# Kernel optimization log

Hardware: AMD Instinct MI355X
Metric: run time of the kernel (lower is better)

The kernel has to match this reference:

```python
import jax, jax.numpy as jnp
import numpy as np

IN_DIM, OUT_DIM, EDGE_DIM = 128, 128, 16
N_NODES, N_EDGES = 20000, 640000


def setup_inputs() -> dict:
    key = jax.random.key(0)
    ks = jax.random.split(key, 16)
    s = lambda fan_in: 1.0 / np.sqrt(fan_in)
    h = jax.random.normal(ks[0], (N_NODES, IN_DIM), dtype=jnp.float32)
    edge_index = jax.random.randint(ks[1], (2, N_EDGES), 0, N_NODES, dtype=jnp.int32)
    edge_attr = jax.random.normal(ks[2], (N_EDGES, EDGE_DIM), dtype=jnp.float32)
    flags = jnp.ones((N_NODES, 1), dtype=jnp.float32)
    edge_mask = jnp.ones((N_EDGES, 1), dtype=jnp.float32)
    din_msg = 2 * IN_DIM + EDGE_DIM
    din_node = IN_DIM + OUT_DIM
    params = {
        'W_m1': jax.random.uniform(ks[3], (din_msg, OUT_DIM), jnp.float32, -s(din_msg), s(din_msg)),
        'b_m1': jnp.zeros((OUT_DIM,), jnp.float32),
        'W_m2': jax.random.uniform(ks[4], (OUT_DIM, OUT_DIM), jnp.float32, -s(OUT_DIM), s(OUT_DIM)),
        'b_m2': jnp.zeros((OUT_DIM,), jnp.float32),
        'W_a': jax.random.uniform(ks[5], (OUT_DIM, 1), jnp.float32, -s(OUT_DIM), s(OUT_DIM)),
        'b_a': jnp.zeros((1,), jnp.float32),
        'W_n1': jax.random.uniform(ks[6], (din_node, OUT_DIM), jnp.float32, -s(din_node), s(din_node)),
        'b_n1': jnp.zeros((OUT_DIM,), jnp.float32),
        'W_n2': jax.random.uniform(ks[7], (OUT_DIM, OUT_DIM), jnp.float32, -s(OUT_DIM), s(OUT_DIM)),
        'b_n2': jnp.zeros((OUT_DIM,), jnp.float32),
    }
    return {'h': h, 'edge_index': edge_index, 'edge_attr': edge_attr,
            'flags': flags, 'edge_mask': edge_mask, **params}


def reference(h, edge_index, edge_attr, flags, edge_mask,
              W_m1, b_m1, W_m2, b_m2, W_a, b_a, W_n1, b_n1, W_n2, b_n2):
    row, col = edge_index[0], edge_index[1]
    # gather endpoints and run edge MLP
    msg = jnp.concatenate([h[row], h[col], edge_attr], axis=1)  # [E, 2*in+edge]
    msg = jax.nn.silu(msg @ W_m1 + b_m1)
    msg = jax.nn.silu(msg @ W_m2 + b_m2)                        # [E, out]
    att = jax.nn.sigmoid(msg @ W_a + b_a)                       # [E, 1]
    msg = msg * att * edge_mask
    # scatter-add into source nodes (aggregation 'sum', norm factor 1)
    agg = jax.ops.segment_sum(msg, row, num_segments=h.shape[0])  # [N, out]
    agg = jnp.concatenate([h, agg], axis=1)                       # [N, in+out]
    upd = jax.nn.silu(agg @ W_n1 + b_n1) @ W_n2 + b_n2
    return (h + upd) * flags
```

## Files before the change

### kernel.cpp

```cpp
#include <hip/hip_runtime.h>
#include <math.h>

#define E_TOT   640000
#define NN      20000
#define DIM     128
#define EDGE_DIM 16

typedef float f32x4 __attribute__((ext_vector_type(4)));
typedef float f32x2 __attribute__((ext_vector_type(2)));
typedef short s16x8 __attribute__((ext_vector_type(8)));
typedef unsigned u32x4 __attribute__((ext_vector_type(4)));
typedef __bf16 bfx8 __attribute__((ext_vector_type(8)));

__device__ __forceinline__ unsigned short f2bf(float f) {
    unsigned u = __builtin_bit_cast(unsigned, f);
    u += 0x7fffu + ((u >> 16) & 1u);
    return (unsigned short)(u >> 16);
}
__device__ __forceinline__ unsigned cvt_pk_bf16(float lo, float hi) {
    unsigned r;
    asm("v_cvt_pk_bf16_f32 %0, %1, %2" : "=v"(r) : "v"(lo), "v"(hi));
    return r;
}
__device__ __forceinline__ float bf_lo(unsigned u) {
    return __builtin_bit_cast(float, u << 16);
}
__device__ __forceinline__ float bf_hi(unsigned u) {
    return __builtin_bit_cast(float, u & 0xffff0000u);
}
__device__ __forceinline__ f32x2 bf2(unsigned u) {
    f32x2 r; r.x = bf_lo(u); r.y = bf_hi(u); return r;
}
__device__ __forceinline__ float fast_exp2(float x) {
    float r; asm("v_exp_f32 %0, %1" : "=v"(r) : "v"(x)); return r;
}
__device__ __forceinline__ float fast_rcp(float x) {
    float r; asm("v_rcp_f32 %0, %1" : "=v"(r) : "v"(x)); return r;
}
#define LOG2E 1.44269504f
__device__ __forceinline__ float silu_f(float x) {
    return x * fast_rcp(1.0f + fast_exp2(-LOG2E * x));
}
__device__ __forceinline__ float sigmoid_f(float x) {
    return fast_rcp(1.0f + fast_exp2(-LOG2E * x));
}
__device__ __forceinline__ f32x2 silu2(f32x2 x) {
    f32x2 nx = x * (-LOG2E);
    f32x2 e; e.x = fast_exp2(nx.x); e.y = fast_exp2(nx.y);
    f32x2 d = e + 1.0f;
    f32x2 rc; rc.x = fast_rcp(d.x); rc.y = fast_rcp(d.y);
    return x * rc;
}

#define MFMA16(a, b, c) __builtin_amdgcn_mfma_f32_16x16x32_bf16( \
    __builtin_bit_cast(bfx8, (a)), __builtin_bit_cast(bfx8, (b)), (c), 0, 0, 0)

__device__ __forceinline__ void pack_w(const float* __restrict__ W,
                                       unsigned short* __restrict__ Wp,
                                       int K, int id) {
    int t   = id & 7;
    int pos = (id >> 3) & 127;
    int sg  = id >> 10;
    int qq = pos & 15, f = pos >> 4;
    int col = (f >> 1) * 32 + 2 * qq + (f & 1);
    int k = sg * 8 + t;
    Wp[id] = (k < K) ? f2bf(W[(size_t)k * DIM + col]) : (unsigned short)0;
}

__global__ void prep_all_kernel(const float* __restrict__ h,
                                unsigned short* __restrict__ h_bf,
                                const float* __restrict__ Wm1,
                                const float* __restrict__ Wm2,
                                const float* __restrict__ Wn1,
                                const float* __restrict__ Wn2,
                                unsigned short* __restrict__ W1rp,
                                unsigned short* __restrict__ W1cp,
                                unsigned short* __restrict__ W1ep,
                                unsigned short* __restrict__ W2p,
                                unsigned short* __restrict__ Wn1p,
                                unsigned short* __restrict__ Wn2p,
                                float* __restrict__ agg,
                                int* __restrict__ cnts) {
    const int blk = blockIdx.x;
    const int tid = threadIdx.x;
    if (blk < 2500) {
        int i = blk * 256 + tid;
        float4 v = reinterpret_cast<const float4*>(h)[i];
        unsigned short* d = h_bf + i * 4;
        d[0] = f2bf(v.x); d[1] = f2bf(v.y); d[2] = f2bf(v.z); d[3] = f2bf(v.w);
    } else if (blk < 2564) {
        pack_w(Wm1, W1rp, 128, (blk - 2500) * 256 + tid);
    } else if (blk < 2628) {
        pack_w(Wm1 + 128 * DIM, W1cp, 128, (blk - 2564) * 256 + tid);
    } else if (blk < 2644) {
        pack_w(Wm1 + 256 * DIM, W1ep, 16, (blk - 2628) * 256 + tid);
    } else if (blk < 2708) {
        pack_w(Wm2, W2p, 128, (blk - 2644) * 256 + tid);
    } else if (blk < 2836) {
        pack_w(Wn1, Wn1p, 256, (blk - 2708) * 256 + tid);
    } else if (blk < 2900) {
        pack_w(Wn2, Wn2p, 128, (blk - 2836) * 256 + tid);
    } else if (blk < 5400) {
        int i = (blk - 2900) * 256 + tid;
        reinterpret_cast<f32x4*>(agg)[i] = (f32x4)0.f;
    } else {
        int i = (blk - 5400) * 256 + tid;
        if (i < NN) cnts[i] = 0;
    }
}

template<bool SORTED>
__global__ __launch_bounds__(256) void hist_proj_kernel(
    const int* __restrict__ ei, int* __restrict__ cnts,
    const unsigned short* __restrict__ h_bf,
    const unsigned short* __restrict__ W1rp,
    const unsigned short* __restrict__ W1cp,
    unsigned* __restrict__ P1r, unsigned* __restrict__ P1c)
{
    const int blk = blockIdx.x;
    const int tid = threadIdx.x;

    if (SORTED && blk < 2500) {
        int e = blk * 256 + tid;
        if (e < E_TOT) atomicAdd(&cnts[ei[e]], 1);
        return;
    }

    const int pblk = SORTED ? (blk - 2500) : blk;
    const int wv   = tid >> 6;
    const int lane = tid & 63;
    const int q    = lane & 15;
    const int g    = lane >> 4;
    const int n0w  = pblk * 64 + wv * 16;
    const int nq   = n0w + q;
    const int nqc  = (nq < NN) ? nq : (NN - 1);

    s16x8 av[4];
    #pragma unroll
    for (int s = 0; s < 4; ++s)
        av[s] = *reinterpret_cast<const s16x8*>(
            h_bf + (size_t)nqc * DIM + s * 32 + g * 8);

    #pragma unroll
    for (int T = 0; T < 2; ++T) {
        const unsigned short* Wp = T ? W1cp : W1rp;
        unsigned* P = T ? P1c : P1r;
        f32x4 acc[8];
        #pragma unroll
        for (int f = 0; f < 8; ++f) acc[f] = (f32x4)0.f;
        #pragma unroll
        for (int s = 0; s < 4; ++s)
            #pragma unroll
            for (int f = 0; f < 8; ++f) {
                s16x8 b = *reinterpret_cast<const s16x8*>(
                    Wp + ((s * 4 + g) * DIM + f * 16 + q) * 8);
                acc[f] = MFMA16(av[s], b, acc[f]);
            }
        #pragma unroll
        for (int r = 0; r < 4; ++r) {
            int n = n0w + g * 4 + r;
            if (n < NN) {
                u32x4 o;
                #pragma unroll
                for (int a = 0; a < 4; ++a)
                    o[a] = cvt_pk_bf16(acc[2 * a][r], acc[2 * a + 1][r]);
                *reinterpret_cast<u32x4*>(P + (size_t)n * 64 + q * 4) = o;
            }
        }
    }
}

__global__ __launch_bounds__(1024) void scan_kernel(int* __restrict__ counts) {
    __shared__ int s[1024];
    const int tid = threadIdx.x;
    const int CH = 20;
    int base = tid * CH;
    int loc[CH];
    int sum = 0;
    #pragma unroll
    for (int i = 0; i < CH; ++i) {
        int idx = base + i;
        loc[i] = (idx < NN) ? counts[idx] : 0;
        sum += loc[i];
    }
    s[tid] = sum;
    __syncthreads();
    for (int off = 1; off < 1024; off <<= 1) {
        int v = (tid >= off) ? s[tid - off] : 0;
        __syncthreads();
        s[tid] += v;
        __syncthreads();
    }
    int run = s[tid] - sum;
    #pragma unroll
    for (int i = 0; i < CH; ++i) {
        int idx = base + i;
        if (idx < NN) counts[idx] = run;
        run += loc[i];
    }
}

__global__ void scatter_kernel(const int* __restrict__ ei, int* __restrict__ cursor,
                               int* __restrict__ eidS, unsigned short* __restrict__ rowS) {
    int e = blockIdx.x * blockDim.x + threadIdx.x;
    if (e < E_TOT) {
        int r = ei[e];
        int p = atomicAdd(&cursor[r], 1);
        eidS[p] = e;
        rowS[p] = (unsigned short)r;
    }
}

template<bool SORTED>
__global__ __launch_bounds__(256, 2) void edge_kernel(
    const unsigned* __restrict__ P1r,
    const unsigned* __restrict__ P1c,
    const int* __restrict__ ei,
    const int* __restrict__ eidS,
    const unsigned short* __restrict__ rowS,
    const float* __restrict__ ea,
    const float* __restrict__ emask,
    const unsigned short* __restrict__ W1ep,
    const float* __restrict__ bm1,
    const unsigned short* __restrict__ W2p,
    const float* __restrict__ bm2,
    const float* __restrict__ Wa, const float* __restrict__ ba,
    float* __restrict__ agg)
{
    __shared__ __align__(16) unsigned char s_u[4][16384];

    const int tid  = threadIdx.x;
    const int wv   = tid >> 6;
    const int lane = tid & 63;
    const int q    = lane & 15;
    const int g    = lane >> 4;

    const int nwg = gridDim.x;
    const int xcd = blockIdx.x & 7;
    const int loc = blockIdx.x >> 3;
    const int qq  = nwg >> 3, rr = nwg & 7;
    const int tile = (xcd < rr) ? (xcd * (qq + 1) + loc)
                                : (rr * (qq + 1) + (xcd - rr) * qq + loc);
    const int e0w = tile * 256 + wv * 64;

    const int   eidl = SORTED ? eidS[e0w + lane] : (e0w + lane);
    const int   rowl = SORTED ? (int)rowS[e0w + lane] : ei[eidl];
    const int   coll = ei[E_TOT + eidl];
    const float mskl = emask[eidl];

    const u32x4* P1r4 = reinterpret_cast<const u32x4*>(P1r);
    const u32x4* P1c4 = reinterpret_cast<const u32x4*>(P1c);

    s16x8 eav[4];
    #pragma unroll
    for (int mi = 0; mi < 4; ++mi) {
        int eid = __shfl(eidl, mi * 16 + q);
        eav[mi] = (s16x8)0;
        if (g < 2) {
            const float4* pe = reinterpret_cast<const float4*>(
                ea + (size_t)eid * EDGE_DIM + g * 8);
            float4 u = pe[0], v = pe[1];
            u32x4 pk;
            pk[0] = cvt_pk_bf16(u.x, u.y); pk[1] = cvt_pk_bf16(u.z, u.w);
            pk[2] = cvt_pk_bf16(v.x, v.y); pk[3] = cvt_pk_bf16(v.z, v.w);
            eav[mi] = __builtin_bit_cast(s16x8, pk);
        }
    }

    s16x8 w1e[8];
    #pragma unroll
    for (int f = 0; f < 8; ++f)
        w1e[f] = *reinterpret_cast<const s16x8*>(
            W1ep + ((size_t)g * DIM + f * 16 + q) * 8);

    f32x2 b1v[4];
    #pragma unroll
    for (int a = 0; a < 4; ++a)
        b1v[a] = *reinterpret_cast<const f32x2*>(bm1 + a * 32 + 2 * q);

    unsigned char* sw = s_u[wv];

    u32x4 pr[4], pc[4];
    #pragma unroll
    for (int r = 0; r < 4; ++r) {
        int e = g * 4 + r;
        pr[r] = P1r4[(size_t)__shfl(rowl, e) * 16 + q];
        pc[r] = P1c4[(size_t)__shfl(coll, e) * 16 + q];
    }

    #pragma unroll
    for (int mi = 0; mi < 4; ++mi) {
        f32x4 a1[8];
        #pragma unroll
        for (int f = 0; f < 8; ++f) a1[f] = (f32x4)0.f;
        #pragma unroll
        for (int f = 0; f < 8; ++f) a1[f] = MFMA16(eav[mi], w1e[f], a1[f]);

        u32x4 prn[4], pcn[4];
        if (mi < 3) {
            #pragma unroll
            for (int r = 0; r < 4; ++r) {
                int e = (mi + 1) * 16 + g * 4 + r;
                prn[r] = P1r4[(size_t)__shfl(rowl, e) * 16 + q];
                pcn[r] = P1c4[(size_t)__shfl(coll, e) * 16 + q];
            }
        }

        #pragma unroll
        for (int r = 0; r < 4; ++r) {
            int e = mi * 16 + g * 4 + r;
            unsigned sx = (unsigned)((e & 7) << 4);
            #pragma unroll
            for (int a = 0; a < 4; ++a) {
                f32x2 t; t.x = a1[2 * a][r]; t.y = a1[2 * a + 1][r];
                t = t + bf2(pr[r][a]) + bf2(pc[r][a]) + b1v[a];
                f32x2 s = silu2(t);
                *reinterpret_cast<unsigned*>(
                    sw + e * 256 + ((a * 64 + q * 4) ^ sx)) = cvt_pk_bf16(s.x, s.y);
            }
        }
        #pragma unroll
        for (int r = 0; r < 4; ++r) { pr[r] = prn[r]; pc[r] = pcn[r]; }
    }

    f32x4 acc2[4][8];
    #pragma unroll
    for (int mi = 0; mi < 4; ++mi)
        #pragma unroll
        for (int f = 0; f < 8; ++f) acc2[mi][f] = (f32x4)0.f;

    #pragma unroll
    for (int s = 0; s < 4; ++s) {
        s16x8 bf[8];
        #pragma unroll
        for (int f = 0; f < 8; ++f)
            bf[f] = *reinterpret_cast<const s16x8*>(
                W2p + ((s * 4 + g) * DIM + f * 16 + q) * 8);
        s16x8 av[4];
        #pragma unroll
        for (int mi = 0; mi < 4; ++mi) {
            int e = mi * 16 + q;
            av[mi] = *reinterpret_cast<const s16x8*>(
                sw + e * 256 + ((s * 64 + g * 16) ^ ((q & 7) << 4)));
        }
        #pragma unroll
        for (int mi = 0; mi < 4; ++mi)
            #pragma unroll
            for (int f = 0; f < 8; ++f) acc2[mi][f] = MFMA16(av[mi], bf[f], acc2[mi][f]);
    }

    unsigned* smsg = reinterpret_cast<unsigned*>(sw);
    {
        f32x2 b2v[4], wav[4];
        #pragma unroll
        for (int a = 0; a < 4; ++a) {
            b2v[a] = *reinterpret_cast<const f32x2*>(bm2 + a * 32 + 2 * q);
            wav[a] = *reinterpret_cast<const f32x2*>(Wa  + a * 32 + 2 * q);
        }
        const float ba0 = ba[0];
        #pragma unroll
        for (int mi = 0; mi < 4; ++mi)
            #pragma unroll
            for (int r = 0; r < 4; ++r) {
                f32x2 pd = (f32x2)0.f;
                f32x2 vv[4];
                #pragma unroll
                for (int a = 0; a < 4; ++a) {
                    f32x2 t; t.x = acc2[mi][2 * a][r]; t.y = acc2[mi][2 * a + 1][r];
                    t = t + b2v[a];
                    vv[a] = silu2(t);
                    pd = pd + vv[a] * wav[a];
                }
                float p = pd.x + pd.y;
                p += __shfl_xor(p, 1);
                p += __shfl_xor(p, 2);
                p += __shfl_xor(p, 4);
                p += __shfl_xor(p, 8);
                int e = mi * 16 + g * 4 + r;
                float mk = __shfl(mskl, e);
                float sc = sigmoid_f(p + ba0) * mk;
                unsigned sx = ((unsigned)(e & 4)) << 2;
                #pragma unroll
                for (int a = 0; a < 4; ++a) {
                    f32x2 m = vv[a] * sc;
                    smsg[e * 64 + ((a * 16 + q) ^ sx)] = cvt_pk_bf16(m.x, m.y);
                }
            }
    }

    {
        const int c = lane;
        f32x2 s = (f32x2)0.f;
        int prow = __builtin_amdgcn_readlane(rowl, 0);
        for (int jb = 0; jb < 64; jb += 8) {
            unsigned v[8];
            #pragma unroll
            for (int k = 0; k < 8; ++k)
                v[k] = smsg[(jb + k) * 64 + (c ^ (((jb + k) & 4) << 2))];
            #pragma unroll
            for (int k = 0; k < 8; ++k) {
                int rj = __builtin_amdgcn_readlane(rowl, jb + k);
                if (rj != prow) {
                    float* dst = agg + (size_t)prow * DIM + (c >> 4) * 32 + 2 * (c & 15);
                    atomicAdd(dst, s.x);
                    atomicAdd(dst + 1, s.y);
                    s = (f32x2)0.f; prow = rj;
                }
                s = s + bf2(v[k]);
            }
        }
        float* dst = agg + (size_t)prow * DIM + (c >> 4) * 32 + 2 * (c & 15);
        atomicAdd(dst, s.x);
        atomicAdd(dst + 1, s.y);
    }
}

__global__ __launch_bounds__(256, 4) void node_kernel(
    const unsigned short* __restrict__ h_bf,
    const float* __restrict__ agg,
    const float* __restrict__ h,
    const float* __restrict__ flags,
    const unsigned short* __restrict__ Wn1p,
    const float* __restrict__ bn1,
    const unsigned short* __restrict__ Wn2p,
    const float* __restrict__ bn2,
    float* __restrict__ out)
{
    __shared__ __align__(16) unsigned char s_u[4][4352];

    const int tid  = threadIdx.x;
    const int wv   = tid >> 6;
    const int lane = tid & 63;
    const int q    = lane & 15;
    const int g    = lane >> 4;
    const int n0w  = blockIdx.x * 64 + wv * 16;

    const int nq  = n0w + q;
    const int nqc = (nq < NN) ? nq : (NN - 1);

    float4 au[4], avv[4];
    #pragma unroll
    for (int s = 0; s < 4; ++s) {
        const float4* pa = reinterpret_cast<const float4*>(
            agg + (size_t)nqc * DIM + s * 32 + g * 8);
        au[s] = pa[0]; avv[s] = pa[1];
    }
    s16x8 ah[4];
    #pragma unroll
    for (int s = 0; s < 4; ++s)
        ah[s] = *reinterpret_cast<const s16x8*>(
            h_bf + (size_t)nqc * DIM + s * 32 + g * 8);

    f32x4 acc[8];
    #pragma unroll
    for (int f = 0; f < 8; ++f) acc[f] = (f32x4)0.f;

    #pragma unroll
    for (int s = 0; s < 4; ++s) {
        #pragma unroll
        for (int f = 0; f < 8; ++f) {
            s16x8 b = *reinterpret_cast<const s16x8*>(
                Wn1p + ((s * 4 + g) * DIM + f * 16 + q) * 8);
            acc[f] = MFMA16(ah[s], b, acc[f]);
        }
    }
    #pragma unroll
    for (int s = 4; s < 8; ++s) {
        float4 u = au[s - 4], v = avv[s - 4];
        u32x4 pk;
        pk[0] = cvt_pk_bf16(u.x, u.y); pk[1] = cvt_pk_bf16(u.z, u.w);
        pk[2] = cvt_pk_bf16(v.x, v.y); pk[3] = cvt_pk_bf16(v.z, v.w);
        s16x8 a = __builtin_bit_cast(s16x8, pk);
        #pragma unroll
        for (int f = 0; f < 8; ++f) {
            s16x8 b = *reinterpret_cast<const s16x8*>(
                Wn1p + ((s * 4 + g) * DIM + f * 16 + q) * 8);
            acc[f] = MFMA16(a, b, acc[f]);
        }
    }

    unsigned char* sw = s_u[wv];
    {
        #pragma unroll
        for (int aa = 0; aa < 4; ++aa) {
            f32x2 bp = *reinterpret_cast<const f32x2*>(bn1 + aa * 32 + 2 * q);
            #pragma unroll
            for (int r = 0; r < 4; ++r) {
                f32x2 t; t.x = acc[2 * aa][r]; t.y = acc[2 * aa + 1][r];
                f32x2 s = silu2(t + bp);
                *reinterpret_cast<unsigned*>(
                    sw + (g * 4 + r) * 272 + aa * 64 + 4 * q) = cvt_pk_bf16(s.x, s.y);
            }
        }
    }

    f32x4 acc2[8];
    #pragma unroll
    for (int f = 0; f < 8; ++f) acc2[f] = (f32x4)0.f;

    #pragma unroll
    for (int s = 0; s < 4; ++s) {
        s16x8 a = *reinterpret_cast<const s16x8*>(sw + q * 272 + s * 64 + g * 16);
        #pragma unroll
        for (int f = 0; f < 8; ++f) {
            s16x8 b = *reinterpret_cast<const s16x8*>(
                Wn2p + ((s * 4 + g) * DIM + f * 16 + q) * 8);
            acc2[f] = MFMA16(a, b, acc2[f]);
        }
    }

    {
        #pragma unroll
        for (int r = 0; r < 4; ++r) {
            int n = n0w + 4 * g + r;
            if (n < NN) {
                float fl = flags[n];
                #pragma unroll
                for (int aa = 0; aa < 4; ++aa) {
                    f32x2 b2 = *reinterpret_cast<const f32x2*>(bn2 + aa * 32 + 2 * q);
                    size_t b = (size_t)n * DIM + aa * 32 + 2 * q;
                    f32x2 hv = *reinterpret_cast<const f32x2*>(h + b);
                    f32x2 t; t.x = acc2[2 * aa][r]; t.y = acc2[2 * aa + 1][r];
                    f32x2 o = (hv + t + b2) * fl;
                    *reinterpret_cast<f32x2*>(out + b) = o;
                }
            }
        }
    }
}

extern "C" void kernel_launch(void* const* d_in, const int* in_sizes, int n_in,
                              void* d_out, int out_size, void* d_ws, size_t ws_size,
                              hipStream_t stream) {
    const float* h     = (const float*)d_in[0];
    const int*   ei    = (const int*)  d_in[1];
    const float* ea    = (const float*)d_in[2];
    const float* flags = (const float*)d_in[3];
    const float* emask = (const float*)d_in[4];
    const float* Wm1   = (const float*)d_in[5];
    const float* bm1   = (const float*)d_in[6];
    const float* Wm2   = (const float*)d_in[7];
    const float* bm2   = (const float*)d_in[8];
    const float* Wa    = (const float*)d_in[9];
    const float* ba    = (const float*)d_in[10];
    const float* Wn1   = (const float*)d_in[11];
    const float* bn1   = (const float*)d_in[12];
    const float* Wn2   = (const float*)d_in[13];
    const float* bn2   = (const float*)d_in[14];
    float* out = (float*)d_out;

    char* ws = (char*)d_ws;
    float*          agg   = (float*)         (ws);
    unsigned short* h_bf  = (unsigned short*)(ws + 10240000);
    unsigned short* W1rp  = (unsigned short*)(ws + 15360000);
    unsigned short* W1cp  = (unsigned short*)(ws + 15392768);
    unsigned short* W1ep  = (unsigned short*)(ws + 15425536);
    unsigned short* W2p   = (unsigned short*)(ws + 15433728);
    unsigned short* Wn1p  = (unsigned short*)(ws + 15466496);
    unsigned short* Wn2p  = (unsigned short*)(ws + 15532032);
    int*            cnts  = (int*)           (ws + 15564800);
    int*            eidS  = (int*)           (ws + 15644800);
    unsigned short* rowS  = (unsigned short*)(ws + 18204800);
    unsigned*       P1r   = (unsigned*)      (ws + 19484800);
    unsigned*       P1c   = (unsigned*)      (ws + 24604800);
    const size_t WS_NEED = 29724800;

    const bool sorted = (ws_size >= WS_NEED);

    prep_all_kernel<<<5479, 256, 0, stream>>>(h, h_bf, Wm1, Wm2, Wn1, Wn2,
                                              W1rp, W1cp, W1ep, W2p, Wn1p, Wn2p,
                                              agg, cnts);

    if (sorted) {
        hist_proj_kernel<true><<<2813, 256, 0, stream>>>(
            ei, cnts, h_bf, W1rp, W1cp, P1r, P1c);
        scan_kernel<<<1, 1024, 0, stream>>>(cnts);
        scatter_kernel<<<(E_TOT + 255) / 256, 256, 0, stream>>>(ei, cnts, eidS, rowS);
        edge_kernel<true><<<E_TOT / 256, 256, 0, stream>>>(
            P1r, P1c, ei, eidS, rowS, ea, emask, W1ep, bm1, W2p, bm2, Wa, ba, agg);
    } else {
        hist_proj_kernel<false><<<313, 256, 0, stream>>>(
            ei, cnts, h_bf, W1rp, W1cp, P1r, P1c);
        edge_kernel<false><<<E_TOT / 256, 256, 0, stream>>>(
            P1r, P1c, ei, eidS, rowS, ea, emask, W1ep, bm1, W2p, bm2, Wa, ba, agg);
    }

    node_kernel<<<(NN + 63) / 64, 256, 0, stream>>>(h_bf, agg, h, flags,
                                                    Wn1p, bn1, Wn2p, bn2, out);
}
```

Before: 227.7 us.

## Fuse histogram into pack, fuse scatter into projection, split node kernel waves

New measurement: 262.1 us. 15.1% more time.

```diff
diff --git a/kernel.cpp b/kernel.cpp
--- a/kernel.cpp
+++ b/kernel.cpp
@@ -38,9 +38,6 @@
     float r; asm("v_rcp_f32 %0, %1" : "=v"(r) : "v"(x)); return r;
 }
 #define LOG2E 1.44269504f
-__device__ __forceinline__ float silu_f(float x) {
-    return x * fast_rcp(1.0f + fast_exp2(-LOG2E * x));
-}
 __device__ __forceinline__ float sigmoid_f(float x) {
     return fast_rcp(1.0f + fast_exp2(-LOG2E * x));
 }
@@ -67,27 +64,24 @@
     Wp[id] = (k < K) ? f2bf(W[(size_t)k * DIM + col]) : (unsigned short)0;
 }
 
-__global__ void prep_all_kernel(const float* __restrict__ h,
-                                unsigned short* __restrict__ h_bf,
-                                const float* __restrict__ Wm1,
-                                const float* __restrict__ Wm2,
-                                const float* __restrict__ Wn1,
-                                const float* __restrict__ Wn2,
-                                unsigned short* __restrict__ W1rp,
-                                unsigned short* __restrict__ W1cp,
-                                unsigned short* __restrict__ W1ep,
-                                unsigned short* __restrict__ W2p,
-                                unsigned short* __restrict__ Wn1p,
-                                unsigned short* __restrict__ Wn2p,
-                                float* __restrict__ agg,
-                                int* __restrict__ cnts) {
+__global__ void hist_pack_kernel(const int* __restrict__ ei,
+                                 int* __restrict__ cnts,
+                                 const float* __restrict__ Wm1,
+                                 const float* __restrict__ Wm2,
+                                 const float* __restrict__ Wn1,
+                                 const float* __restrict__ Wn2,
+                                 unsigned short* __restrict__ W1rp,
+                                 unsigned short* __restrict__ W1cp,
+                                 unsigned short* __restrict__ W1ep,
+                                 unsigned short* __restrict__ W2p,
+                                 unsigned short* __restrict__ Wn1p,
+                                 unsigned short* __restrict__ Wn2p,
+                                 float* __restrict__ agg) {
     const int blk = blockIdx.x;
     const int tid = threadIdx.x;
     if (blk < 2500) {
-        int i = blk * 256 + tid;
-        float4 v = reinterpret_cast<const float4*>(h)[i];
-        unsigned short* d = h_bf + i * 4;
-        d[0] = f2bf(v.x); d[1] = f2bf(v.y); d[2] = f2bf(v.z); d[3] = f2bf(v.w);
+        int e = blk * 256 + tid;
+        if (e < E_TOT) atomicAdd(&cnts[ei[e]], 1);
     } else if (blk < 2564) {
         pack_w(Wm1, W1rp, 128, (blk - 2500) * 256 + tid);
     } else if (blk < 2628) {
@@ -100,19 +94,48 @@
         pack_w(Wn1, Wn1p, 256, (blk - 2708) * 256 + tid);
     } else if (blk < 2900) {
         pack_w(Wn2, Wn2p, 128, (blk - 2836) * 256 + tid);
-    } else if (blk < 5400) {
+    } else {
         int i = (blk - 2900) * 256 + tid;
         reinterpret_cast<f32x4*>(agg)[i] = (f32x4)0.f;
-    } else {
-        int i = (blk - 5400) * 256 + tid;
-        if (i < NN) cnts[i] = 0;
+    }
+}
+
+__global__ __launch_bounds__(1024) void scan_kernel(int* __restrict__ counts) {
+    __shared__ int s[1024];
+    const int tid = threadIdx.x;
+    const int CH = 20;
+    int base = tid * CH;
+    int loc[CH];
+    int sum = 0;
+    #pragma unroll
+    for (int i = 0; i < CH; ++i) {
+        int idx = base + i;
+        loc[i] = (idx < NN) ? counts[idx] : 0;
+        sum += loc[i];
+    }
+    s[tid] = sum;
+    __syncthreads();
+    for (int off = 1; off < 1024; off <<= 1) {
+        int v = (tid >= off) ? s[tid - off] : 0;
+        __syncthreads();
+        s[tid] += v;
+        __syncthreads();
+    }
+    int run = s[tid] - sum;
+    #pragma unroll
+    for (int i = 0; i < CH; ++i) {
+        int idx = base + i;
+        if (idx < NN) counts[idx] = run;
+        run += loc[i];
     }
 }
 
 template<bool SORTED>
-__global__ __launch_bounds__(256) void hist_proj_kernel(
-    const int* __restrict__ ei, int* __restrict__ cnts,
-    const unsigned short* __restrict__ h_bf,
+__global__ __launch_bounds__(256) void prep_scatter_proj_kernel(
+    const float* __restrict__ h,
+    unsigned short* __restrict__ h_bf,
+    const int* __restrict__ ei, int* __restrict__ cursor,
+    int* __restrict__ eidS, unsigned short* __restrict__ rowS,
     const unsigned short* __restrict__ W1rp,
     const unsigned short* __restrict__ W1cp,
     unsigned* __restrict__ P1r, unsigned* __restrict__ P1c)
@@ -120,13 +143,25 @@
     const int blk = blockIdx.x;
     const int tid = threadIdx.x;
 
-    if (SORTED && blk < 2500) {
-        int e = blk * 256 + tid;
-        if (e < E_TOT) atomicAdd(&cnts[ei[e]], 1);
+    if (blk < 2500) {
+        int i = blk * 256 + tid;
+        float4 v = reinterpret_cast<const float4*>(h)[i];
+        unsigned short* d = h_bf + i * 4;
+        d[0] = f2bf(v.x); d[1] = f2bf(v.y); d[2] = f2bf(v.z); d[3] = f2bf(v.w);
         return;
     }
-
-    const int pblk = SORTED ? (blk - 2500) : blk;
+    if (SORTED && blk < 5000) {
+        int e = (blk - 2500) * 256 + tid;
+        if (e < E_TOT) {
+            int r = ei[e];
+            int p = atomicAdd(&cursor[r], 1);
+            eidS[p] = e;
+            rowS[p] = (unsigned short)r;
+        }
+        return;
+    }
+
+    const int pblk = SORTED ? (blk - 5000) : (blk - 2500);
     const int wv   = tid >> 6;
     const int lane = tid & 63;
     const int q    = lane & 15;
@@ -137,9 +172,15 @@
 
     s16x8 av[4];
     #pragma unroll
-    for (int s = 0; s < 4; ++s)
-        av[s] = *reinterpret_cast<const s16x8*>(
-            h_bf + (size_t)nqc * DIM + s * 32 + g * 8);
+    for (int s = 0; s < 4; ++s) {
+        const float4* ph = reinterpret_cast<const float4*>(
+            h + (size_t)nqc * DIM + s * 32 + g * 8);
+        float4 u = ph[0], v = ph[1];
+        u32x4 pk;
+        pk[0] = cvt_pk_bf16(u.x, u.y); pk[1] = cvt_pk_bf16(u.z, u.w);
+        pk[2] = cvt_pk_bf16(v.x, v.y); pk[3] = cvt_pk_bf16(v.z, v.w);
+        av[s] = __builtin_bit_cast(s16x8, pk);
+    }
 
     #pragma unroll
     for (int T = 0; T < 2; ++T) {
@@ -167,47 +208,6 @@
                 *reinterpret_cast<u32x4*>(P + (size_t)n * 64 + q * 4) = o;
             }
         }
-    }
-}
-
-__global__ __launch_bounds__(1024) void scan_kernel(int* __restrict__ counts) {
-    __shared__ int s[1024];
-    const int tid = threadIdx.x;
-    const int CH = 20;
-    int base = tid * CH;
-    int loc[CH];
-    int sum = 0;
-    #pragma unroll
-    for (int i = 0; i < CH; ++i) {
-        int idx = base + i;
-        loc[i] = (idx < NN) ? counts[idx] : 0;
-        sum += loc[i];
-    }
-    s[tid] = sum;
-    __syncthreads();
-    for (int off = 1; off < 1024; off <<= 1) {
-        int v = (tid >= off) ? s[tid - off] : 0;
-        __syncthreads();
-        s[tid] += v;
-        __syncthreads();
-    }
-    int run = s[tid] - sum;
-    #pragma unroll
-    for (int i = 0; i < CH; ++i) {
-        int idx = base + i;
-        if (idx < NN) counts[idx] = run;
-        run += loc[i];
-    }
-}
-
-__global__ void scatter_kernel(const int* __restrict__ ei, int* __restrict__ cursor,
-                               int* __restrict__ eidS, unsigned short* __restrict__ rowS) {
-    int e = blockIdx.x * blockDim.x + threadIdx.x;
-    if (e < E_TOT) {
-        int r = ei[e];
-        int p = atomicAdd(&cursor[r], 1);
-        eidS[p] = e;
-        rowS[p] = (unsigned short)r;
     }
 }
 
@@ -251,6 +251,16 @@
     const u32x4* P1r4 = reinterpret_cast<const u32x4*>(P1r);
     const u32x4* P1c4 = reinterpret_cast<const u32x4*>(P1c);
 
+    u32x4 pr[4][4], pc[4][4];
+    #pragma unroll
+    for (int mi = 0; mi < 4; ++mi)
+        #pragma unroll
+        for (int r = 0; r < 4; ++r) {
+            int e = mi * 16 + g * 4 + r;
+            pr[mi][r] = P1r4[(size_t)__shfl(rowl, e) * 16 + q];
+            pc[mi][r] = P1c4[(size_t)__shfl(coll, e) * 16 + q];
+        }
+
     s16x8 eav[4];
     #pragma unroll
     for (int mi = 0; mi < 4; ++mi) {
@@ -280,14 +290,6 @@
 
     unsigned char* sw = s_u[wv];
 
-    u32x4 pr[4], pc[4];
-    #pragma unroll
-    for (int r = 0; r < 4; ++r) {
-        int e = g * 4 + r;
-        pr[r] = P1r4[(size_t)__shfl(rowl, e) * 16 + q];
-        pc[r] = P1c4[(size_t)__shfl(coll, e) * 16 + q];
-    }
-
     #pragma unroll
     for (int mi = 0; mi < 4; ++mi) {
         f32x4 a1[8];
@@ -295,16 +297,6 @@
         for (int f = 0; f < 8; ++f) a1[f] = (f32x4)0.f;
         #pragma unroll
         for (int f = 0; f < 8; ++f) a1[f] = MFMA16(eav[mi], w1e[f], a1[f]);
-
-        u32x4 prn[4], pcn[4];
-        if (mi < 3) {
-            #pragma unroll
-            for (int r = 0; r < 4; ++r) {
-                int e = (mi + 1) * 16 + g * 4 + r;
-                prn[r] = P1r4[(size_t)__shfl(rowl, e) * 16 + q];
-                pcn[r] = P1c4[(size_t)__shfl(coll, e) * 16 + q];
-            }
-        }
 
         #pragma unroll
         for (int r = 0; r < 4; ++r) {
@@ -313,14 +305,12 @@
             #pragma unroll
             for (int a = 0; a < 4; ++a) {
                 f32x2 t; t.x = a1[2 * a][r]; t.y = a1[2 * a + 1][r];
-                t = t + bf2(pr[r][a]) + bf2(pc[r][a]) + b1v[a];
+                t = t + bf2(pr[mi][r][a]) + bf2(pc[mi][r][a]) + b1v[a];
                 f32x2 s = silu2(t);
                 *reinterpret_cast<unsigned*>(
                     sw + e * 256 + ((a * 64 + q * 4) ^ sx)) = cvt_pk_bf16(s.x, s.y);
             }
         }
-        #pragma unroll
-        for (int r = 0; r < 4; ++r) { pr[r] = prn[r]; pc[r] = pcn[r]; }
     }
 
     f32x4 acc2[4][8];
@@ -426,14 +416,16 @@
     const float* __restrict__ bn2,
     float* __restrict__ out)
 {
-    __shared__ __align__(16) unsigned char s_u[4][4352];
+    __shared__ __align__(16) unsigned char s_u[2][4352];
 
     const int tid  = threadIdx.x;
     const int wv   = tid >> 6;
     const int lane = tid & 63;
     const int q    = lane & 15;
     const int g    = lane >> 4;
-    const int n0w  = blockIdx.x * 64 + wv * 16;
+    const int grp  = wv >> 1;
+    const int half = wv & 1;
+    const int n0w  = blockIdx.x * 32 + grp * 16;
 
     const int nq  = n0w + q;
     const int nqc = (nq < NN) ? nq : (NN - 1);
@@ -451,16 +443,16 @@
         ah[s] = *reinterpret_cast<const s16x8*>(
             h_bf + (size_t)nqc * DIM + s * 32 + g * 8);
 
-    f32x4 acc[8];
-    #pragma unroll
-    for (int f = 0; f < 8; ++f) acc[f] = (f32x4)0.f;
+    f32x4 acc[4];
+    #pragma unroll
+    for (int f = 0; f < 4; ++f) acc[f] = (f32x4)0.f;
 
     #pragma unroll
     for (int s = 0; s < 4; ++s) {
         #pragma unroll
-        for (int f = 0; f < 8; ++f) {
+        for (int f = 0; f < 4; ++f) {
             s16x8 b = *reinterpret_cast<const s16x8*>(
-                Wn1p + ((s * 4 + g) * DIM + f * 16 + q) * 8);
+                Wn1p + ((s * 4 + g) * DIM + (half * 4 + f) * 16 + q) * 8);
             acc[f] = MFMA16(ah[s], b, acc[f]);
         }
     }
@@ -472,39 +464,41 @@
         pk[2] = cvt_pk_bf16(v.x, v.y); pk[3] = cvt_pk_bf16(v.z, v.w);
         s16x8 a = __builtin_bit_cast(s16x8, pk);
         #pragma unroll
-        for (int f = 0; f < 8; ++f) {
+        for (int f = 0; f < 4; ++f) {
             s16x8 b = *reinterpret_cast<const s16x8*>(
-                Wn1p + ((s * 4 + g) * DIM + f * 16 + q) * 8);
+                Wn1p + ((s * 4 + g) * DIM + (half * 4 + f) * 16 + q) * 8);
             acc[f] = MFMA16(a, b, acc[f]);
         }
     }
 
-    unsigned char* sw = s_u[wv];
+    unsigned char* sg_ = s_u[grp];
     {
         #pragma unroll
-        for (int aa = 0; aa < 4; ++aa) {
+        for (int a = 0; a < 2; ++a) {
+            int aa = half * 2 + a;
             f32x2 bp = *reinterpret_cast<const f32x2*>(bn1 + aa * 32 + 2 * q);
             #pragma unroll
             for (int r = 0; r < 4; ++r) {
-                f32x2 t; t.x = acc[2 * aa][r]; t.y = acc[2 * aa + 1][r];
+                f32x2 t; t.x = acc[2 * a][r]; t.y = acc[2 * a + 1][r];
                 f32x2 s = silu2(t + bp);
                 *reinterpret_cast<unsigned*>(
-                    sw + (g * 4 + r) * 272 + aa * 64 + 4 * q) = cvt_pk_bf16(s.x, s.y);
-            }
-        }
-    }
-
-    f32x4 acc2[8];
-    #pragma unroll
-    for (int f = 0; f < 8; ++f) acc2[f] = (f32x4)0.f;
+                    sg_ + (g * 4 + r) * 272 + aa * 64 + 4 * q) = cvt_pk_bf16(s.x, s.y);
+            }
+        }
+    }
+    __syncthreads();
+
+    f32x4 acc2[4];
+    #pragma unroll
+    for (int f = 0; f < 4; ++f) acc2[f] = (f32x4)0.f;
 
     #pragma unroll
     for (int s = 0; s < 4; ++s) {
-        s16x8 a = *reinterpret_cast<const s16x8*>(sw + q * 272 + s * 64 + g * 16);
-        #pragma unroll
-        for (int f = 0; f < 8; ++f) {
+        s16x8 a = *reinterpret_cast<const s16x8*>(sg_ + q * 272 + s * 64 + g * 16);
+        #pragma unroll
+        for (int f = 0; f < 4; ++f) {
             s16x8 b = *reinterpret_cast<const s16x8*>(
-                Wn2p + ((s * 4 + g) * DIM + f * 16 + q) * 8);
+                Wn2p + ((s * 4 + g) * DIM + (half * 4 + f) * 16 + q) * 8);
             acc2[f] = MFMA16(a, b, acc2[f]);
         }
     }
@@ -516,11 +510,12 @@
             if (n < NN) {
                 float fl = flags[n];
                 #pragma unroll
-                for (int aa = 0; aa < 4; ++aa) {
+                for (int a = 0; a < 2; ++a) {
+                    int aa = half * 2 + a;
                     f32x2 b2 = *reinterpret_cast<const f32x2*>(bn2 + aa * 32 + 2 * q);
                     size_t b = (size_t)n * DIM + aa * 32 + 2 * q;
                     f32x2 hv = *reinterpret_cast<const f32x2*>(h + b);
-                    f32x2 t; t.x = acc2[2 * aa][r]; t.y = acc2[2 * aa + 1][r];
+                    f32x2 t; t.x = acc2[2 * a][r]; t.y = acc2[2 * a + 1][r];
                     f32x2 o = (hv + t + b2) * fl;
                     *reinterpret_cast<f32x2*>(out + b) = o;
                 }
@@ -567,24 +562,27 @@
 
     const bool sorted = (ws_size >= WS_NEED);
 
-    prep_all_kernel<<<5479, 256, 0, stream>>>(h, h_bf, Wm1, Wm2, Wn1, Wn2,
-                                              W1rp, W1cp, W1ep, W2p, Wn1p, Wn2p,
-                                              agg, cnts);
-
     if (sorted) {
-        hist_proj_kernel<true><<<2813, 256, 0, stream>>>(
-            ei, cnts, h_bf, W1rp, W1cp, P1r, P1c);
+        hipMemsetAsync(cnts, 0, NN * sizeof(int), stream);
+        hist_pack_kernel<<<5400, 256, 0, stream>>>(
+            ei, cnts, Wm1, Wm2, Wn1, Wn2,
+            W1rp, W1cp, W1ep, W2p, Wn1p, Wn2p, agg);
         scan_kernel<<<1, 1024, 0, stream>>>(cnts);
-        scatter_kernel<<<(E_TOT + 255) / 256, 256, 0, stream>>>(ei, cnts, eidS, rowS);
+        prep_scatter_proj_kernel<true><<<5313, 256, 0, stream>>>(
+            h, h_bf, ei, cnts, eidS, rowS, W1rp, W1cp, P1r, P1c);
         edge_kernel<true><<<E_TOT / 256, 256, 0, stream>>>(
             P1r, P1c, ei, eidS, rowS, ea, emask, W1ep, bm1, W2p, bm2, Wa, ba, agg);
     } else {
-        hist_proj_kernel<false><<<313, 256, 0, stream>>>(
-            ei, cnts, h_bf, W1rp, W1cp, P1r, P1c);
+        hipMemsetAsync(cnts, 0, NN * sizeof(int), stream);
+        hist_pack_kernel<<<5400, 256, 0, stream>>>(
+            ei, cnts, Wm1, Wm2, Wn1, Wn2,
+            W1rp, W1cp, W1ep, W2p, Wn1p, Wn2p, agg);
+        prep_scatter_proj_kernel<false><<<2813, 256, 0, stream>>>(
+            h, h_bf, ei, cnts, eidS, rowS, W1rp, W1cp, P1r, P1c);
         edge_kernel<false><<<E_TOT / 256, 256, 0, stream>>>(
             P1r, P1c, ei, eidS, rowS, ea, emask, W1ep, bm1, W2p, bm2, Wa, ba, agg);
     }
 
-    node_kernel<<<(NN + 63) / 64, 256, 0, stream>>>(h_bf, agg, h, flags,
+    node_kernel<<<(NN + 31) / 32, 256, 0, stream>>>(h_bf, agg, h, flags,
                                                     Wn1p, bn1, Wn2p, bn2, out);
 }
```

## Reshuffle prep stages: fold histogram into weight-pack kernel, fuse scan with projection

Applied to the files above, without the earlier changes.

Result: faster. 220.0 us (-3.4%).

```diff
diff --git a/kernel.cpp b/kernel.cpp
--- a/kernel.cpp
+++ b/kernel.cpp
@@ -38,9 +38,6 @@
     float r; asm("v_rcp_f32 %0, %1" : "=v"(r) : "v"(x)); return r;
 }
 #define LOG2E 1.44269504f
-__device__ __forceinline__ float silu_f(float x) {
-    return x * fast_rcp(1.0f + fast_exp2(-LOG2E * x));
-}
 __device__ __forceinline__ float sigmoid_f(float x) {
     return fast_rcp(1.0f + fast_exp2(-LOG2E * x));
 }
@@ -67,27 +64,24 @@
     Wp[id] = (k < K) ? f2bf(W[(size_t)k * DIM + col]) : (unsigned short)0;
 }
 
-__global__ void prep_all_kernel(const float* __restrict__ h,
-                                unsigned short* __restrict__ h_bf,
-                                const float* __restrict__ Wm1,
-                                const float* __restrict__ Wm2,
-                                const float* __restrict__ Wn1,
-                                const float* __restrict__ Wn2,
-                                unsigned short* __restrict__ W1rp,
-                                unsigned short* __restrict__ W1cp,
-                                unsigned short* __restrict__ W1ep,
-                                unsigned short* __restrict__ W2p,
-                                unsigned short* __restrict__ Wn1p,
-                                unsigned short* __restrict__ Wn2p,
-                                float* __restrict__ agg,
-                                int* __restrict__ cnts) {
+__global__ void hist_pack_kernel(const int* __restrict__ ei,
+                                 int* __restrict__ cnts,
+                                 const float* __restrict__ Wm1,
+                                 const float* __restrict__ Wm2,
+                                 const float* __restrict__ Wn1,
+                                 const float* __restrict__ Wn2,
+                                 unsigned short* __restrict__ W1rp,
+                                 unsigned short* __restrict__ W1cp,
+                                 unsigned short* __restrict__ W1ep,
+                                 unsigned short* __restrict__ W2p,
+                                 unsigned short* __restrict__ Wn1p,
+                                 unsigned short* __restrict__ Wn2p,
+                                 float* __restrict__ agg) {
     const int blk = blockIdx.x;
     const int tid = threadIdx.x;
     if (blk < 2500) {
-        int i = blk * 256 + tid;
-        float4 v = reinterpret_cast<const float4*>(h)[i];
-        unsigned short* d = h_bf + i * 4;
-        d[0] = f2bf(v.x); d[1] = f2bf(v.y); d[2] = f2bf(v.z); d[3] = f2bf(v.w);
+        int e = blk * 256 + tid;
+        if (e < E_TOT) atomicAdd(&cnts[ei[e]], 1);
     } else if (blk < 2564) {
         pack_w(Wm1, W1rp, 128, (blk - 2500) * 256 + tid);
     } else if (blk < 2628) {
@@ -100,19 +94,17 @@
         pack_w(Wn1, Wn1p, 256, (blk - 2708) * 256 + tid);
     } else if (blk < 2900) {
         pack_w(Wn2, Wn2p, 128, (blk - 2836) * 256 + tid);
-    } else if (blk < 5400) {
+    } else {
         int i = (blk - 2900) * 256 + tid;
         reinterpret_cast<f32x4*>(agg)[i] = (f32x4)0.f;
-    } else {
-        int i = (blk - 5400) * 256 + tid;
-        if (i < NN) cnts[i] = 0;
     }
 }
 
 template<bool SORTED>
-__global__ __launch_bounds__(256) void hist_proj_kernel(
-    const int* __restrict__ ei, int* __restrict__ cnts,
-    const unsigned short* __restrict__ h_bf,
+__global__ __launch_bounds__(1024) void scan_preph_proj_kernel(
+    int* __restrict__ counts,
+    const float* __restrict__ h,
+    unsigned short* __restrict__ h_bf,
     const unsigned short* __restrict__ W1rp,
     const unsigned short* __restrict__ W1cp,
     unsigned* __restrict__ P1r, unsigned* __restrict__ P1c)
@@ -120,26 +112,65 @@
     const int blk = blockIdx.x;
     const int tid = threadIdx.x;
 
-    if (SORTED && blk < 2500) {
-        int e = blk * 256 + tid;
-        if (e < E_TOT) atomicAdd(&cnts[ei[e]], 1);
+    if (SORTED && blk == 0) {
+        __shared__ int s[1024];
+        const int CH = 20;
+        int base = tid * CH;
+        int loc[CH];
+        int sum = 0;
+        #pragma unroll
+        for (int i = 0; i < CH; ++i) {
+            int idx = base + i;
+            loc[i] = (idx < NN) ? counts[idx] : 0;
+            sum += loc[i];
+        }
+        s[tid] = sum;
+        __syncthreads();
+        for (int off = 1; off < 1024; off <<= 1) {
+            int v = (tid >= off) ? s[tid - off] : 0;
+            __syncthreads();
+            s[tid] += v;
+            __syncthreads();
+        }
+        int run = s[tid] - sum;
+        #pragma unroll
+        for (int i = 0; i < CH; ++i) {
+            int idx = base + i;
+            if (idx < NN) counts[idx] = run;
+            run += loc[i];
+        }
         return;
     }
 
-    const int pblk = SORTED ? (blk - 2500) : blk;
+    const int pb = SORTED ? blk : (blk + 1);
+    if (pb < 626) {
+        int i = (pb - 1) * 1024 + tid;
+        float4 v = reinterpret_cast<const float4*>(h)[i];
+        unsigned short* d = h_bf + i * 4;
+        d[0] = f2bf(v.x); d[1] = f2bf(v.y); d[2] = f2bf(v.z); d[3] = f2bf(v.w);
+        return;
+    }
+
+    const int pblk = pb - 626;
     const int wv   = tid >> 6;
     const int lane = tid & 63;
     const int q    = lane & 15;
     const int g    = lane >> 4;
-    const int n0w  = pblk * 64 + wv * 16;
+    const int n0w  = pblk * 256 + wv * 16;
     const int nq   = n0w + q;
     const int nqc  = (nq < NN) ? nq : (NN - 1);
 
     s16x8 av[4];
     #pragma unroll
-    for (int s = 0; s < 4; ++s)
-        av[s] = *reinterpret_cast<const s16x8*>(
-            h_bf + (size_t)nqc * DIM + s * 32 + g * 8);
+    for (int s = 0; s < 4; ++s) {
+        const float4* ph = reinterpret_cast<const float4*>(
+            h + (size_t)nqc * DIM + s * 32 + g * 8);
+        float4 u = ph[0], v = ph[1];
+        unsigned short tmp[8];
+        tmp[0] = f2bf(u.x); tmp[1] = f2bf(u.y); tmp[2] = f2bf(u.z); tmp[3] = f2bf(u.w);
+        tmp[4] = f2bf(v.x); tmp[5] = f2bf(v.y); tmp[6] = f2bf(v.z); tmp[7] = f2bf(v.w);
+        av[s] = *reinterpret_cast<const s16x8*>(tmp);
+    }
 
     #pragma unroll
     for (int T = 0; T < 2; ++T) {
@@ -167,36 +198,6 @@
                 *reinterpret_cast<u32x4*>(P + (size_t)n * 64 + q * 4) = o;
             }
         }
-    }
-}
-
-__global__ __launch_bounds__(1024) void scan_kernel(int* __restrict__ counts) {
-    __shared__ int s[1024];
-    const int tid = threadIdx.x;
-    const int CH = 20;
-    int base = tid * CH;
-    int loc[CH];
-    int sum = 0;
-    #pragma unroll
-    for (int i = 0; i < CH; ++i) {
-        int idx = base + i;
-        loc[i] = (idx < NN) ? counts[idx] : 0;
-        sum += loc[i];
-    }
-    s[tid] = sum;
-    __syncthreads();
-    for (int off = 1; off < 1024; off <<= 1) {
-        int v = (tid >= off) ? s[tid - off] : 0;
-        __syncthreads();
-        s[tid] += v;
-        __syncthreads();
-    }
-    int run = s[tid] - sum;
-    #pragma unroll
-    for (int i = 0; i < CH; ++i) {
-        int idx = base + i;
-        if (idx < NN) counts[idx] = run;
-        run += loc[i];
     }
 }
 
@@ -567,20 +568,20 @@
 
     const bool sorted = (ws_size >= WS_NEED);
 
-    prep_all_kernel<<<5479, 256, 0, stream>>>(h, h_bf, Wm1, Wm2, Wn1, Wn2,
-                                              W1rp, W1cp, W1ep, W2p, Wn1p, Wn2p,
-                                              agg, cnts);
+    hipMemsetAsync(cnts, 0, NN * sizeof(int), stream);
+    hist_pack_kernel<<<5400, 256, 0, stream>>>(
+        ei, cnts, Wm1, Wm2, Wn1, Wn2,
+        W1rp, W1cp, W1ep, W2p, Wn1p, Wn2p, agg);
 
     if (sorted) {
-        hist_proj_kernel<true><<<2813, 256, 0, stream>>>(
-            ei, cnts, h_bf, W1rp, W1cp, P1r, P1c);
-        scan_kernel<<<1, 1024, 0, stream>>>(cnts);
+        scan_preph_proj_kernel<true><<<705, 1024, 0, stream>>>(
+            cnts, h, h_bf, W1rp, W1cp, P1r, P1c);
         scatter_kernel<<<(E_TOT + 255) / 256, 256, 0, stream>>>(ei, cnts, eidS, rowS);
         edge_kernel<true><<<E_TOT / 256, 256, 0, stream>>>(
             P1r, P1c, ei, eidS, rowS, ea, emask, W1ep, bm1, W2p, bm2, Wa, ba, agg);
     } else {
-        hist_proj_kernel<false><<<313, 256, 0, stream>>>(
-            ei, cnts, h_bf, W1rp, W1cp, P1r, P1c);
+        scan_preph_proj_kernel<false><<<704, 1024, 0, stream>>>(
+            cnts, h, h_bf, W1rp, W1cp, P1r, P1c);
         edge_kernel<false><<<E_TOT / 256, 256, 0, stream>>>(
             P1r, P1c, ei, eidS, rowS, ea, emask, W1ep, bm1, W2p, bm2, Wa, ba, agg);
     }
```
